# Kernel optimization log

Hardware: AMD Instinct MI355X
Metric: run time of the kernel (lower is better)

## Reference

```python
import jax, jax.numpy as jnp
import numpy as np

B, S, D, H = 4, 2048, 1024, 16
HD = D // H  # head_size = 64


def setup_inputs() -> dict:
    key = jax.random.key(0)
    ks = jax.random.split(key, 8)
    scale = 1.0 / np.sqrt(D)
    return {
        "q": jax.random.normal(ks[0], (B, S, D), dtype=jnp.float32),
        "k": jax.random.normal(ks[1], (B, S, D), dtype=jnp.float32),
        "v": jax.random.normal(ks[2], (B, S, D), dtype=jnp.float32),
        "mask": jnp.ones((B, 1, S, S), dtype=jnp.int32),
        "W_q": jax.random.normal(ks[3], (D, D), dtype=jnp.float32) * scale,
        "W_k": jax.random.normal(ks[4], (D, D), dtype=jnp.float32) * scale,
        "W_v": jax.random.normal(ks[5], (D, D), dtype=jnp.float32) * scale,
        "W_o": jax.random.normal(ks[6], (D, D), dtype=jnp.float32) * scale,
    }


def reference(q, k, v, mask, W_q, W_k, W_v, W_o):
    # Linear projections (nn.Linear with bias=False: x @ W.T; here W stored as (D_out, D_in))
    query = q @ W_q.T  # (B,S,D)
    key_ = k @ W_k.T
    value = v @ W_v.T
    # split heads -> (B,H,S,hd)
    query = query.reshape(B, S, H, HD).transpose(0, 2, 1, 3)
    key_ = key_.reshape(B, S, H, HD).transpose(0, 2, 1, 3)
    value = value.reshape(B, S, H, HD).transpose(0, 2, 1, 3)
    # scaled dot-product attention, materializing full (B,H,S,S) scores as original does
    att = jnp.einsum('bhqd,bhkd->bhqk', query, key_) * (HD ** -0.5)
    att = jnp.where(mask == 0, -jnp.inf, att)
    att = jax.nn.softmax(att, axis=-1)
    y = jnp.einsum('bhqk,bhkd->bhqd', att, value)
    y = y.transpose(0, 2, 1, 3).reshape(B, S, D)
    return y @ W_o.T
```

## Files before the change

### kernel.cpp

```cpp
#include <hip/hip_runtime.h>
#include <stdint.h>

#define B_ 4
#define S_ 2048
#define D_ 1024
#define H_ 16
#define HD_ 64
#define K_ 1024
#define N_ 1024

typedef __attribute__((ext_vector_type(8))) short short8;
typedef __attribute__((ext_vector_type(4))) float f32x4;
typedef __attribute__((ext_vector_type(16))) float f32x16;

#define MFMA16(a,b,c) __builtin_amdgcn_mfma_f32_16x16x32_bf16((a),(b),(c),0,0,0)
#define MFMA32(a,b,c) __builtin_amdgcn_mfma_f32_32x32x16_bf16((a),(b),(c),0,0,0)

__device__ __forceinline__ unsigned short f2bf(float f) {
  union { float f; uint32_t u; } v; v.f = f;
  uint32_t u = v.u;
  u += 0x7fffu + ((u >> 16) & 1u);
  return (unsigned short)(u >> 16);
}

__device__ __forceinline__ uint32_t cvtpk(float lo, float hi) {
  uint32_t r;
  asm("v_cvt_pk_bf16_f32 %0, %1, %2" : "=v"(r) : "v"(lo), "v"(hi));
  return r;
}

__device__ __forceinline__ void pl32swap(uint32_t &a, uint32_t &b) {
#if __has_builtin(__builtin_amdgcn_permlane32_swap)
  typedef __attribute__((ext_vector_type(2))) int i32x2;
  i32x2 r = __builtin_amdgcn_permlane32_swap((int)a, (int)b, false, false);
  a = (uint32_t)r[0]; b = (uint32_t)r[1];
#else
  asm volatile("s_nop 1\n\tv_permlane32_swap_b32 %0, %1\n\ts_nop 1" : "+v"(a), "+v"(b));
#endif
}

__device__ __forceinline__ float fexp2(float x) {
#if __has_builtin(__builtin_amdgcn_exp2f)
  return __builtin_amdgcn_exp2f(x);
#else
  return exp2f(x);
#endif
}

typedef __attribute__((address_space(1))) const uint32_t gbl_u32;
typedef __attribute__((address_space(3))) uint32_t lds_u32;

__device__ __forceinline__ void gload_lds16(const void* g, void* l) {
  __builtin_amdgcn_global_load_lds((gbl_u32*)g, (lds_u32*)l, 16, 0, 0);
}

__global__ __launch_bounds__(256)
void cvt_qkv(const float* __restrict__ q, const float* __restrict__ k, const float* __restrict__ v,
             unsigned short* __restrict__ qo, unsigned short* __restrict__ ko, unsigned short* __restrict__ vo)
{
  const float* s; unsigned short* d;
  if (blockIdx.z == 0)      { s = q; d = qo; }
  else if (blockIdx.z == 1) { s = k; d = ko; }
  else                      { s = v; d = vo; }
  const size_t i = ((size_t)blockIdx.x * 256 + threadIdx.x) * 4;
  const float4 f = *(const float4*)(s + i);
  ushort4 o;
  o.x = f2bf(f.x); o.y = f2bf(f.y); o.z = f2bf(f.z); o.w = f2bf(f.w);
  *(ushort4*)(d + i) = o;
}

__global__ __launch_bounds__(256)
void cvt_w(const float* __restrict__ a, const float* __restrict__ b,
           const float* __restrict__ c, const float* __restrict__ dd,
           unsigned short* __restrict__ ao, unsigned short* __restrict__ bo,
           unsigned short* __restrict__ co, unsigned short* __restrict__ eo)
{
  const float* s; unsigned short* d;
  switch (blockIdx.z) {
    case 0:  s = a;  d = ao; break;
    case 1:  s = b;  d = bo; break;
    case 2:  s = c;  d = co; break;
    default: s = dd; d = eo; break;
  }
  const size_t i = ((size_t)blockIdx.x * 256 + threadIdx.x) * 4;
  const float4 f = *(const float4*)(s + i);
  ushort4 o;
  o.x = f2bf(f.x); o.y = f2bf(f.y); o.z = f2bf(f.z); o.w = f2bf(f.w);
  *(ushort4*)(d + i) = o;
}

template<int EPI>
__global__ __launch_bounds__(256)
void gemm_bt(const unsigned short* __restrict__ A, const unsigned short* __restrict__ Bt,
             float* __restrict__ Cf, unsigned short* __restrict__ Cb, float scale)
{
  __shared__ unsigned short As[128 * 64];
  __shared__ unsigned short Bs[128 * 64];
  const int tid  = threadIdx.x;
  const int lane = tid & 63, wave = tid >> 6;
  const int r15 = lane & 15, g = lane >> 4;
  const int sw = (r15 & 7) << 4;
  const int m0 = blockIdx.y * 128, n0 = blockIdx.x * 128;
  const int wm = (wave >> 1) * 64, wn = (wave & 1) * 64;
  f32x4 acc[4][4] = {};
  const char* AsB = (const char*)As;
  const char* BsB = (const char*)Bs;

  for (int kt = 0; kt < K_; kt += 64) {
    #pragma unroll
    for (int i = 0; i < 4; ++i) {
      const int off  = i * 4096 + tid * 16;
      const int row  = off >> 7;
      const int srcb = (off & 127) ^ ((row & 7) << 4);
      const int col  = kt + (srcb >> 1);
      gload_lds16(A  + (size_t)(m0 + row) * K_ + col, (char*)As + off);
      gload_lds16(Bt + (size_t)(n0 + row) * K_ + col, (char*)Bs + off);
    }
    __syncthreads();
    #pragma unroll
    for (int kc = 0; kc < 2; ++kc) {
      short8 af[4], bfr[4];
      #pragma unroll
      for (int mf = 0; mf < 4; ++mf)
        af[mf] = *(const short8*)(AsB + (wm + mf*16 + r15) * 128 + ((kc*64 + g*16) ^ sw));
      #pragma unroll
      for (int nf = 0; nf < 4; ++nf)
        bfr[nf] = *(const short8*)(BsB + (wn + nf*16 + r15) * 128 + ((kc*64 + g*16) ^ sw));
      #pragma unroll
      for (int mf = 0; mf < 4; ++mf)
        #pragma unroll
        for (int nf = 0; nf < 4; ++nf)
          acc[mf][nf] = MFMA16(af[mf], bfr[nf], acc[mf][nf]);
    }
    __syncthreads();
  }

  #pragma unroll
  for (int mf = 0; mf < 4; ++mf) {
    #pragma unroll
    for (int nf = 0; nf < 4; ++nf) {
      const int col   = n0 + wn + nf*16 + r15;
      const int rbase = m0 + wm + mf*16 + g*4;
      if constexpr (EPI == 0) {
        #pragma unroll
        for (int r = 0; r < 4; ++r)
          Cf[(size_t)(rbase + r) * N_ + col] = acc[mf][nf][r] * scale;
      } else if constexpr (EPI == 1) {
        const int hh = col >> 6, dd = col & 63;
        #pragma unroll
        for (int r = 0; r < 4; ++r) {
          const int row = rbase + r;
          const int bb = row >> 11, ss = row & (S_ - 1);
          Cb[(((size_t)(bb * H_ + hh)) * S_ + ss) * HD_ + dd] = f2bf(acc[mf][nf][r] * scale);
        }
      } else {
        const int hh = col >> 6, dd = col & 63;
        const int bb = rbase >> 11, ss = rbase & (S_ - 1);
        ushort4 o;
        o.x = f2bf(acc[mf][nf][0] * scale);
        o.y = f2bf(acc[mf][nf][1] * scale);
        o.z = f2bf(acc[mf][nf][2] * scale);
        o.w = f2bf(acc[mf][nf][3] * scale);
        *(ushort4*)&Cb[(((size_t)(bb * H_ + hh)) * HD_ + dd) * S_ + ss] = o;
      }
    }
  }
}

__global__ __launch_bounds__(256)
void attn(const unsigned short* __restrict__ Qp, const unsigned short* __restrict__ Kp,
          const unsigned short* __restrict__ Vt, unsigned short* __restrict__ Y)
{
  __shared__ unsigned short Ks[64 * 64];
  __shared__ unsigned short Vs[64 * 64];
  const int tid  = threadIdx.x;
  const int lane = tid & 63, wave = tid >> 6;
  const int l31 = lane & 31, h = lane >> 5;
  const int sw = (l31 & 7) << 4;
  const int bh = blockIdx.y, bb = bh >> 4, hh = bh & 15;
  const int q0w = blockIdx.x * 128 + wave * 32;
  const size_t qkbase = (size_t)bh * (S_ * HD_);
  const size_t vtbase = (size_t)bh * (HD_ * S_);
  const char* KsB = (const char*)Ks;
  const char* VsB = (const char*)Vs;

  short8 qf[4];
  #pragma unroll
  for (int sl = 0; sl < 4; ++sl)
    qf[sl] = *(const short8*)&Qp[qkbase + (size_t)(q0w + l31) * HD_ + sl*16 + h*8];

  f32x16 yA = {0,0,0,0,0,0,0,0,0,0,0,0,0,0,0,0};
  f32x16 yB = {0,0,0,0,0,0,0,0,0,0,0,0,0,0,0,0};
  float mrun = -__builtin_inff(), lrun = 0.f;

  for (int k0 = 0; k0 < S_; k0 += 64) {
    #pragma unroll
    for (int i = 0; i < 2; ++i) {
      const int off  = i * 4096 + tid * 16;
      const int row  = off >> 7;
      const int srcb = (off & 127) ^ ((row & 7) << 4);
      gload_lds16(&Kp[qkbase + (size_t)(k0 + row) * HD_ + (srcb >> 1)], (char*)Ks + off);
      gload_lds16(&Vt[vtbase + (size_t)row * S_ + k0 + (srcb >> 1)],    (char*)Vs + off);
    }
    __syncthreads();

    f32x16 sc0 = {0,0,0,0,0,0,0,0,0,0,0,0,0,0,0,0};
    f32x16 sc1 = {0,0,0,0,0,0,0,0,0,0,0,0,0,0,0,0};
    __builtin_amdgcn_s_setprio(1);
    #pragma unroll
    for (int sl = 0; sl < 4; ++sl) {
      const int colb = (sl*32 + h*16) ^ sw;
      const short8 ka0 = *(const short8*)(KsB + l31*128 + colb);
      const short8 ka1 = *(const short8*)(KsB + (32 + l31)*128 + colb);
      sc0 = MFMA32(ka0, qf[sl], sc0);
      sc1 = MFMA32(ka1, qf[sl], sc1);
    }
    __builtin_amdgcn_s_setprio(0);

    float t[16];
    #pragma unroll
    for (int r = 0; r < 16; ++r) t[r] = fmaxf(sc0[r], sc1[r]);
    #pragma unroll
    for (int r = 0; r < 8; ++r) t[r] = fmaxf(t[r], t[r+8]);
    #pragma unroll
    for (int r = 0; r < 4; ++r) t[r] = fmaxf(t[r], t[r+4]);
    t[0] = fmaxf(fmaxf(t[0], t[1]), fmaxf(t[2], t[3]));
    float pmax = fmaxf(t[0], __shfl_xor(t[0], 32));

    if (!__all(pmax <= mrun + 8.0f)) {
      const float mnew  = fmaxf(mrun, pmax);
      const float alpha = fexp2(mrun - mnew);
      mrun = mnew;
      #pragma unroll
      for (int r = 0; r < 16; ++r) { yA[r] *= alpha; yB[r] *= alpha; }
      lrun *= alpha;
    }
    #pragma unroll
    for (int r = 0; r < 16; ++r) {
      sc0[r] = fexp2(sc0[r] - mrun);
      sc1[r] = fexp2(sc1[r] - mrun);
    }
    float s[16];
    #pragma unroll
    for (int r = 0; r < 16; ++r) s[r] = sc0[r] + sc1[r];
    #pragma unroll
    for (int r = 0; r < 8; ++r) s[r] += s[r+8];
    #pragma unroll
    for (int r = 0; r < 4; ++r) s[r] += s[r+4];
    float rs = (s[0] + s[1]) + (s[2] + s[3]);
    rs += __shfl_xor(rs, 32);
    lrun += rs;

    uint32_t pf[4][4];
    #pragma unroll
    for (int ks = 0; ks < 4; ++ks) {
      const f32x16& sv = (ks < 2) ? sc0 : sc1;
      const int rb = (ks & 1) * 8;
      uint32_t x0 = cvtpk(sv[rb+0], sv[rb+1]);
      uint32_t x1 = cvtpk(sv[rb+2], sv[rb+3]);
      uint32_t y0 = cvtpk(sv[rb+4], sv[rb+5]);
      uint32_t y1 = cvtpk(sv[rb+6], sv[rb+7]);
      pl32swap(x0, y0);
      pl32swap(x1, y1);
      pf[ks][0] = x0; pf[ks][1] = x1; pf[ks][2] = y0; pf[ks][3] = y1;
    }

    __builtin_amdgcn_s_setprio(1);
    #pragma unroll
    for (int ks = 0; ks < 4; ++ks) {
      union { uint32_t u[4]; short8 v; } pu;
      pu.u[0] = pf[ks][0]; pu.u[1] = pf[ks][1]; pu.u[2] = pf[ks][2]; pu.u[3] = pf[ks][3];
      const int colb = (ks*32 + h*16) ^ sw;
      const short8 va0 = *(const short8*)(VsB + l31*128 + colb);
      const short8 va1 = *(const short8*)(VsB + (32 + l31)*128 + colb);
      yA = MFMA32(va0, pu.v, yA);
      yB = MFMA32(va1, pu.v, yB);
    }
    __builtin_amdgcn_s_setprio(0);
    __syncthreads();
  }

  const float inv = 1.0f / lrun;
  const int qg = q0w + l31;
  unsigned short* Yrow = &Y[((size_t)(bb * S_ + qg)) * D_ + hh * HD_];
  #pragma unroll
  for (int tq = 0; tq < 4; ++tq) {
    ushort4 oa, ob;
    oa.x = f2bf(yA[4*tq+0] * inv); oa.y = f2bf(yA[4*tq+1] * inv);
    oa.z = f2bf(yA[4*tq+2] * inv); oa.w = f2bf(yA[4*tq+3] * inv);
    ob.x = f2bf(yB[4*tq+0] * inv); ob.y = f2bf(yB[4*tq+1] * inv);
    ob.z = f2bf(yB[4*tq+2] * inv); ob.w = f2bf(yB[4*tq+3] * inv);
    const int d = 8*tq + 4*h;
    *(ushort4*)&Yrow[d]      = oa;
    *(ushort4*)&Yrow[32 + d] = ob;
  }
}

extern "C" void kernel_launch(void* const* d_in, const int* in_sizes, int n_in,
                              void* d_out, int out_size, void* d_ws, size_t ws_size,
                              hipStream_t stream)
{
  const float* q  = (const float*)d_in[0];
  const float* k  = (const float*)d_in[1];
  const float* v  = (const float*)d_in[2];
  const float* Wq = (const float*)d_in[4];
  const float* Wk = (const float*)d_in[5];
  const float* Wv = (const float*)d_in[6];
  const float* Wo = (const float*)d_in[7];
  float* out = (float*)d_out;
  char* ws = (char*)d_ws;

  unsigned short* qb  = (unsigned short*)(ws + 0);
  unsigned short* kb  = (unsigned short*)(ws + (16u << 20));
  unsigned short* vb  = (unsigned short*)(ws + (32u << 20));
  unsigned short* Wqb = (unsigned short*)(ws + (48u << 20));
  unsigned short* Wkb = (unsigned short*)(ws + (50u << 20));
  unsigned short* Wvb = (unsigned short*)(ws + (52u << 20));
  unsigned short* Wob = (unsigned short*)(ws + (54u << 20));
  unsigned short* Qp  = (unsigned short*)(ws + (56u << 20));
  unsigned short* Kp  = (unsigned short*)(ws + (72u << 20));
  unsigned short* Vt  = (unsigned short*)(ws + (88u << 20));
  unsigned short* Yb  = qb;

  dim3 blk(256, 1, 1);
  cvt_qkv<<<dim3(8192, 1, 3), blk, 0, stream>>>(q, k, v, qb, kb, vb);
  cvt_w  <<<dim3(1024, 1, 4), blk, 0, stream>>>(Wq, Wk, Wv, Wo, Wqb, Wkb, Wvb, Wob);
  gemm_bt<1><<<dim3(8, 64, 1), blk, 0, stream>>>(qb, Wqb, nullptr, Qp, 0.18033688f);
  gemm_bt<1><<<dim3(8, 64, 1), blk, 0, stream>>>(kb, Wkb, nullptr, Kp, 1.0f);
  gemm_bt<2><<<dim3(8, 64, 1), blk, 0, stream>>>(vb, Wvb, nullptr, Vt, 1.0f);
  attn<<<dim3(16, 64, 1), blk, 0, stream>>>(Qp, Kp, Vt, Yb);
  gemm_bt<0><<<dim3(8, 64, 1), blk, 0, stream>>>(Yb, Wob, out, nullptr, 1.0f);

  (void)in_sizes; (void)n_in; (void)out_size; (void)ws_size;
}
```

Baseline: 388.3 us.

## Double-buffer K/V tiles in attention and swizzle block order for L2 locality

The attention kernel now keeps two LDS buffers for K and V and issues the global-to-LDS loads for the next tile before computing on the current one, so memory latency can overlap the MFMA and softmax work. Both the GEMM and attention kernels remap the flat block index so that consecutively scheduled blocks spread across XCD-sized groups, aiming for better L2 reuse. The double buffering doubles LDS use per block, which may lower occupancy. It also depends on the trailing __syncthreads to guarantee the async loads have landed before the buffer is read.

```diff
diff --git a/kernel.cpp b/kernel.cpp
--- a/kernel.cpp
+++ b/kernel.cpp
@@ -73,7 +73,7 @@
 void cvt_w(const float* __restrict__ a, const float* __restrict__ b,
            const float* __restrict__ c, const float* __restrict__ dd,
            unsigned short* __restrict__ ao, unsigned short* __restrict__ bo,
-           unsigned short* __restrict__ co, unsigned short* __restrict__ eo)
+             unsigned short* __restrict__ co, unsigned short* __restrict__ eo)
 {
   const float* s; unsigned short* d;
   switch (blockIdx.z) {
@@ -100,7 +100,9 @@
   const int lane = tid & 63, wave = tid >> 6;
   const int r15 = lane & 15, g = lane >> 4;
   const int sw = (r15 & 7) << 4;
-  const int m0 = blockIdx.y * 128, n0 = blockIdx.x * 128;
+  const int flat = blockIdx.x + blockIdx.y * 8;
+  const int swzb = (flat & 7) * 64 + (flat >> 3);
+  const int m0 = (swzb >> 3) * 128, n0 = (swzb & 7) * 128;
   const int wm = (wave >> 1) * 64, wn = (wave & 1) * 64;
   f32x4 acc[4][4] = {};
   const char* AsB = (const char*)As;
@@ -171,18 +173,19 @@
 void attn(const unsigned short* __restrict__ Qp, const unsigned short* __restrict__ Kp,
           const unsigned short* __restrict__ Vt, unsigned short* __restrict__ Y)
 {
-  __shared__ unsigned short Ks[64 * 64];
-  __shared__ unsigned short Vs[64 * 64];
+  __shared__ unsigned short Ks[2][64 * 64];
+  __shared__ unsigned short Vs[2][64 * 64];
   const int tid  = threadIdx.x;
   const int lane = tid & 63, wave = tid >> 6;
   const int l31 = lane & 31, h = lane >> 5;
   const int sw = (l31 & 7) << 4;
-  const int bh = blockIdx.y, bb = bh >> 4, hh = bh & 15;
-  const int q0w = blockIdx.x * 128 + wave * 32;
+  const int flat = blockIdx.x + blockIdx.y * 16;
+  const int swzb = (flat & 7) * 128 + (flat >> 3);
+  const int qblk = swzb & 15, bh = swzb >> 4;
+  const int bb = bh >> 4, hh = bh & 15;
+  const int q0w = qblk * 128 + wave * 32;
   const size_t qkbase = (size_t)bh * (S_ * HD_);
   const size_t vtbase = (size_t)bh * (HD_ * S_);
-  const char* KsB = (const char*)Ks;
-  const char* VsB = (const char*)Vs;
 
   short8 qf[4];
   #pragma unroll
@@ -193,16 +196,31 @@
   f32x16 yB = {0,0,0,0,0,0,0,0,0,0,0,0,0,0,0,0};
   float mrun = -__builtin_inff(), lrun = 0.f;
 
+  #pragma unroll
+  for (int i = 0; i < 2; ++i) {
+    const int off  = i * 4096 + tid * 16;
+    const int row  = off >> 7;
+    const int srcb = (off & 127) ^ ((row & 7) << 4);
+    gload_lds16(&Kp[qkbase + (size_t)row * HD_ + (srcb >> 1)], (char*)Ks[0] + off);
+    gload_lds16(&Vt[vtbase + (size_t)row * S_ + (srcb >> 1)],  (char*)Vs[0] + off);
+  }
+  __syncthreads();
+
+  int buf = 0;
   for (int k0 = 0; k0 < S_; k0 += 64) {
-    #pragma unroll
-    for (int i = 0; i < 2; ++i) {
-      const int off  = i * 4096 + tid * 16;
-      const int row  = off >> 7;
-      const int srcb = (off & 127) ^ ((row & 7) << 4);
-      gload_lds16(&Kp[qkbase + (size_t)(k0 + row) * HD_ + (srcb >> 1)], (char*)Ks + off);
-      gload_lds16(&Vt[vtbase + (size_t)row * S_ + k0 + (srcb >> 1)],    (char*)Vs + off);
-    }
-    __syncthreads();
+    if (k0 + 64 < S_) {
+      const int kn = k0 + 64;
+      #pragma unroll
+      for (int i = 0; i < 2; ++i) {
+        const int off  = i * 4096 + tid * 16;
+        const int row  = off >> 7;
+        const int srcb = (off & 127) ^ ((row & 7) << 4);
+        gload_lds16(&Kp[qkbase + (size_t)(kn + row) * HD_ + (srcb >> 1)], (char*)Ks[buf ^ 1] + off);
+        gload_lds16(&Vt[vtbase + (size_t)row * S_ + kn + (srcb >> 1)],    (char*)Vs[buf ^ 1] + off);
+      }
+    }
+    const char* KsB = (const char*)Ks[buf];
+    const char* VsB = (const char*)Vs[buf];
 
     f32x16 sc0 = {0,0,0,0,0,0,0,0,0,0,0,0,0,0,0,0};
     f32x16 sc1 = {0,0,0,0,0,0,0,0,0,0,0,0,0,0,0,0};
@@ -278,6 +296,7 @@
     }
     __builtin_amdgcn_s_setprio(0);
     __syncthreads();
+    buf ^= 1;
   }
 
   const float inv = 1.0f / lrun;
```

New measurement: 388.0 us. No clear change (-0.1%).

## Merge conversion and QKV projection launches, add XCD-aware block swizzle

Applied to the files above, without the earlier changes.

Fuses the two fp32-to-bf16 conversion kernels into one launch and the three Q/K/V projection GEMMs into one launch indexed by blockIdx.z. It also remaps block indices in the GEMMs and the attention kernel so that consecutive blocks dispatched round-robin across the chip's 8 XCDs share A rows or the same head, improving L2 reuse. This cuts launch gaps and tail effects but adds runtime branching on z and a more complex index computation.

```diff
diff --git a/kernel.cpp b/kernel.cpp
--- a/kernel.cpp
+++ b/kernel.cpp
@@ -55,52 +55,56 @@
 }
 
 __global__ __launch_bounds__(256)
-void cvt_qkv(const float* __restrict__ q, const float* __restrict__ k, const float* __restrict__ v,
-             unsigned short* __restrict__ qo, unsigned short* __restrict__ ko, unsigned short* __restrict__ vo)
-{
-  const float* s; unsigned short* d;
-  if (blockIdx.z == 0)      { s = q; d = qo; }
-  else if (blockIdx.z == 1) { s = k; d = ko; }
-  else                      { s = v; d = vo; }
-  const size_t i = ((size_t)blockIdx.x * 256 + threadIdx.x) * 4;
+void cvt_all(const float* __restrict__ q, const float* __restrict__ k, const float* __restrict__ v,
+             const float* __restrict__ wq, const float* __restrict__ wk,
+             const float* __restrict__ wv, const float* __restrict__ wo,
+             unsigned short* __restrict__ qb, unsigned short* __restrict__ kb,
+             unsigned short* __restrict__ vb, unsigned short* __restrict__ wqb,
+             unsigned short* __restrict__ wkb, unsigned short* __restrict__ wvb,
+             unsigned short* __restrict__ wob)
+{
+  const int b = blockIdx.x;
+  const float* s; unsigned short* d; int local;
+  if (b < 24576) {
+    const int t = b >> 13; local = b & 8191;
+    s = (t == 0) ? q : (t == 1) ? k : v;
+    d = (t == 0) ? qb : (t == 1) ? kb : vb;
+  } else {
+    const int t = (b - 24576) >> 10; local = (b - 24576) & 1023;
+    s = (t == 0) ? wq : (t == 1) ? wk : (t == 2) ? wv : wo;
+    d = (t == 0) ? wqb : (t == 1) ? wkb : (t == 2) ? wvb : wob;
+  }
+  const size_t i = ((size_t)local * 256 + threadIdx.x) * 4;
   const float4 f = *(const float4*)(s + i);
   ushort4 o;
   o.x = f2bf(f.x); o.y = f2bf(f.y); o.z = f2bf(f.z); o.w = f2bf(f.w);
   *(ushort4*)(d + i) = o;
 }
 
+
 __global__ __launch_bounds__(256)
-void cvt_w(const float* __restrict__ a, const float* __restrict__ b,
-           const float* __restrict__ c, const float* __restrict__ dd,
-           unsigned short* __restrict__ ao, unsigned short* __restrict__ bo,
-           unsigned short* __restrict__ co, unsigned short* __restrict__ eo)
-{
-  const float* s; unsigned short* d;
-  switch (blockIdx.z) {
-    case 0:  s = a;  d = ao; break;
-    case 1:  s = b;  d = bo; break;
-    case 2:  s = c;  d = co; break;
-    default: s = dd; d = eo; break;
-  }
-  const size_t i = ((size_t)blockIdx.x * 256 + threadIdx.x) * 4;
-  const float4 f = *(const float4*)(s + i);
-  ushort4 o;
-  o.x = f2bf(f.x); o.y = f2bf(f.y); o.z = f2bf(f.z); o.w = f2bf(f.w);
-  *(ushort4*)(d + i) = o;
-}
-
-template<int EPI>
-__global__ __launch_bounds__(256)
-void gemm_bt(const unsigned short* __restrict__ A, const unsigned short* __restrict__ Bt,
-             float* __restrict__ Cf, unsigned short* __restrict__ Cb, float scale)
+void gemm_proj(const unsigned short* __restrict__ qb, const unsigned short* __restrict__ kb,
+               const unsigned short* __restrict__ vb,
+               const unsigned short* __restrict__ Wqb, const unsigned short* __restrict__ Wkb,
+               const unsigned short* __restrict__ Wvb,
+               unsigned short* __restrict__ Qp, unsigned short* __restrict__ Kp,
+               unsigned short* __restrict__ Vt)
 {
   __shared__ unsigned short As[128 * 64];
   __shared__ unsigned short Bs[128 * 64];
+  const int z = blockIdx.z;
+  const unsigned short* A  = (z == 0) ? qb  : (z == 1) ? kb  : vb;
+  const unsigned short* Bt = (z == 0) ? Wqb : (z == 1) ? Wkb : Wvb;
+  unsigned short* C        = (z == 0) ? Qp  : (z == 1) ? Kp  : Vt;
+  const float scale = (z == 0) ? 0.18033688f : 1.0f;
+
   const int tid  = threadIdx.x;
   const int lane = tid & 63, wave = tid >> 6;
   const int r15 = lane & 15, g = lane >> 4;
   const int sw = (r15 & 7) << 4;
-  const int m0 = blockIdx.y * 128, n0 = blockIdx.x * 128;
+  const int flat = blockIdx.x + blockIdx.y * 8;
+  const int swzb = (flat & 7) * 64 + (flat >> 3);
+  const int m0 = (swzb >> 3) * 128, n0 = (swzb & 7) * 128;
   const int wm = (wave >> 1) * 64, wn = (wave & 1) * 64;
   f32x4 acc[4][4] = {};
   const char* AsB = (const char*)As;
@@ -141,30 +145,84 @@
     for (int nf = 0; nf < 4; ++nf) {
       const int col   = n0 + wn + nf*16 + r15;
       const int rbase = m0 + wm + mf*16 + g*4;
-      if constexpr (EPI == 0) {
-        #pragma unroll
-        for (int r = 0; r < 4; ++r)
-          Cf[(size_t)(rbase + r) * N_ + col] = acc[mf][nf][r] * scale;
-      } else if constexpr (EPI == 1) {
-        const int hh = col >> 6, dd = col & 63;
+      const int hh = col >> 6, dd = col & 63;
+      if (z < 2) {
         #pragma unroll
         for (int r = 0; r < 4; ++r) {
           const int row = rbase + r;
           const int bb = row >> 11, ss = row & (S_ - 1);
-          Cb[(((size_t)(bb * H_ + hh)) * S_ + ss) * HD_ + dd] = f2bf(acc[mf][nf][r] * scale);
+          C[(((size_t)(bb * H_ + hh)) * S_ + ss) * HD_ + dd] = f2bf(acc[mf][nf][r] * scale);
         }
       } else {
-        const int hh = col >> 6, dd = col & 63;
         const int bb = rbase >> 11, ss = rbase & (S_ - 1);
         ushort4 o;
-        o.x = f2bf(acc[mf][nf][0] * scale);
-        o.y = f2bf(acc[mf][nf][1] * scale);
-        o.z = f2bf(acc[mf][nf][2] * scale);
-        o.w = f2bf(acc[mf][nf][3] * scale);
-        *(ushort4*)&Cb[(((size_t)(bb * H_ + hh)) * HD_ + dd) * S_ + ss] = o;
+        o.x = f2bf(acc[mf][nf][0]);
+        o.y = f2bf(acc[mf][nf][1]);
+        o.z = f2bf(acc[mf][nf][2]);
+        o.w = f2bf(acc[mf][nf][3]);
+        *(ushort4*)&C[(((size_t)(bb * H_ + hh)) * HD_ + dd) * S_ + ss] = o;
       }
     }
   }
+}
+
+__global__ __launch_bounds__(256)
+void gemm_out(const unsigned short* __restrict__ A, const unsigned short* __restrict__ Bt,
+              float* __restrict__ Cf)
+{
+  __shared__ unsigned short As[128 * 64];
+  __shared__ unsigned short Bs[128 * 64];
+  const int tid  = threadIdx.x;
+  const int lane = tid & 63, wave = tid >> 6;
+  const int r15 = lane & 15, g = lane >> 4;
+  const int sw = (r15 & 7) << 4;
+  const int flat = blockIdx.x + blockIdx.y * 8;
+  const int swzb = (flat & 7) * 64 + (flat >> 3);
+  const int m0 = (swzb >> 3) * 128, n0 = (swzb & 7) * 128;
+  const int wm = (wave >> 1) * 64, wn = (wave & 1) * 64;
+  f32x4 acc[4][4] = {};
+  const char* AsB = (const char*)As;
+  const char* BsB = (const char*)Bs;
+
+  for (int kt = 0; kt < K_; kt += 64) {
+    #pragma unroll
+    for (int i = 0; i < 4; ++i) {
+      const int off  = i * 4096 + tid * 16;
+      const int row  = off >> 7;
+      const int srcb = (off & 127) ^ ((row & 7) << 4);
+      const int col  = kt + (srcb >> 1);
+      gload_lds16(A  + (size_t)(m0 + row) * K_ + col, (char*)As + off);
+      gload_lds16(Bt + (size_t)(n0 + row) * K_ + col, (char*)Bs + off);
+    }
+    __syncthreads();
+    #pragma unroll
+    for (int kc = 0; kc < 2; ++kc) {
+      short8 af[4], bfr[4];
+      #pragma unroll
+      for (int mf = 0; mf < 4; ++mf)
+        af[mf] = *(const short8*)(AsB + (wm + mf*16 + r15) * 128 + ((kc*64 + g*16) ^ sw));
+      #pragma unroll
+      for (int nf = 0; nf < 4; ++nf)
+        bfr[nf] = *(const short8*)(BsB + (wn + nf*16 + r15) * 128 + ((kc*64 + g*16) ^ sw));
+      #pragma unroll
+      for (int mf = 0; mf < 4; ++mf)
+        #pragma unroll
+        for (int nf = 0; nf < 4; ++nf)
+          acc[mf][nf] = MFMA16(af[mf], bfr[nf], acc[mf][nf]);
+    }
+    __syncthreads();
+  }
+
+  #pragma unroll
+  for (int mf = 0; mf < 4; ++mf)
+    #pragma unroll
+    for (int nf = 0; nf < 4; ++nf) {
+      const int col   = n0 + wn + nf*16 + r15;
+      const int rbase = m0 + wm + mf*16 + g*4;
+      #pragma unroll
+      for (int r = 0; r < 4; ++r)
+        Cf[(size_t)(rbase + r) * N_ + col] = acc[mf][nf][r];
+    }
 }
 
 __global__ __launch_bounds__(256)
@@ -177,8 +235,11 @@
   const int lane = tid & 63, wave = tid >> 6;
   const int l31 = lane & 31, h = lane >> 5;
   const int sw = (l31 & 7) << 4;
-  const int bh = blockIdx.y, bb = bh >> 4, hh = bh & 15;
-  const int q0w = blockIdx.x * 128 + wave * 32;
+  const int flat = blockIdx.x + blockIdx.y * 16;
+  const int swzb = (flat & 7) * 128 + (flat >> 3);
+  const int qblk = swzb & 15, bh = swzb >> 4;
+  const int bb = bh >> 4, hh = bh & 15;
+  const int q0w = qblk * 128 + wave * 32;
   const size_t qkbase = (size_t)bh * (S_ * HD_);
   const size_t vtbase = (size_t)bh * (HD_ * S_);
   const char* KsB = (const char*)Ks;
@@ -323,13 +384,11 @@
   unsigned short* Yb  = qb;
 
   dim3 blk(256, 1, 1);
-  cvt_qkv<<<dim3(8192, 1, 3), blk, 0, stream>>>(q, k, v, qb, kb, vb);
-  cvt_w  <<<dim3(1024, 1, 4), blk, 0, stream>>>(Wq, Wk, Wv, Wo, Wqb, Wkb, Wvb, Wob);
-  gemm_bt<1><<<dim3(8, 64, 1), blk, 0, stream>>>(qb, Wqb, nullptr, Qp, 0.18033688f);
-  gemm_bt<1><<<dim3(8, 64, 1), blk, 0, stream>>>(kb, Wkb, nullptr, Kp, 1.0f);
-  gemm_bt<2><<<dim3(8, 64, 1), blk, 0, stream>>>(vb, Wvb, nullptr, Vt, 1.0f);
+  cvt_all<<<dim3(28672, 1, 1), blk, 0, stream>>>(q, k, v, Wq, Wk, Wv, Wo,
+                                                 qb, kb, vb, Wqb, Wkb, Wvb, Wob);
+  gemm_proj<<<dim3(8, 64, 3), blk, 0, stream>>>(qb, kb, vb, Wqb, Wkb, Wvb, Qp, Kp, Vt);
   attn<<<dim3(16, 64, 1), blk, 0, stream>>>(Qp, Kp, Vt, Yb);
-  gemm_bt<0><<<dim3(8, 64, 1), blk, 0, stream>>>(Yb, Wob, out, nullptr, 1.0f);
+  gemm_out<<<dim3(8, 64, 1), blk, 0, stream>>>(Yb, Wob, out);
 
   (void)in_sizes; (void)n_in; (void)out_size; (void)ws_size;
 }
```

Result: faster. 369.4 us (-4.9%).
